# Kernel optimization log

Hardware: AMD Instinct MI355X
Metric: run time of the kernel (lower is better)

Reference implementation:

```python
import jax, jax.numpy as jnp
import numpy as np

OUT_DIM = 64
N_NODES = 50000
N_EDGES = 1000000


def setup_inputs() -> dict:
    key = jax.random.key(0)
    k1, k2, k3, k4, k5, k6 = jax.random.split(key, 6)
    return {
        "G_h": jax.random.normal(k1, (N_NODES, OUT_DIM), dtype=jnp.float32),
        "K_h": jax.random.normal(k2, (N_NODES, OUT_DIM), dtype=jnp.float32),
        "Q_h": jax.random.normal(k3, (N_NODES, OUT_DIM), dtype=jnp.float32),
        "V_h": jax.random.normal(k4, (N_NODES, 1, OUT_DIM), dtype=jnp.float32),
        "src": jax.random.randint(k5, (N_EDGES,), 0, N_NODES, dtype=jnp.int64),
        "dst": jax.random.randint(k6, (N_EDGES,), 0, N_NODES, dtype=jnp.int64),
    }


def reference(G_h, K_h, Q_h, V_h, src, dst):
    inv_sqrt_d = 1.0 / np.sqrt(OUT_DIM).astype(np.float32)
    # edge-wise gather of node features
    diff = G_h[src] - G_h[dst]                                   # [E, D]
    dist = -jnp.sqrt(jnp.sum(diff * diff, axis=-1) + 1e-6)       # [E]
    distance = jnp.exp(jnp.clip(dist * inv_sqrt_d, -5.0, 5.0))   # [E]
    score = jnp.sum(K_h[src] * Q_h[dst], axis=-1)                # [E]
    score_e = jnp.exp(jnp.clip(score * inv_sqrt_d, -5.0, 5.0))   # [E]
    weight = (score_e * distance)[:, None, None]                 # [E,1,1]
    v1_h = weight * V_h[src]                                     # [E,1,D]
    return v1_h
```

## Files before the change

### kernel.cpp

```cpp
#include <hip/hip_runtime.h>
#include <math.h>

#define N_NODES 50000
#define OUT_DIM 64

typedef float f32x4 __attribute__((ext_vector_type(4)));

__global__ __launch_bounds__(256) void edge_message_kernel(
    const float* __restrict__ G,
    const float* __restrict__ K,
    const float* __restrict__ Q,
    const float* __restrict__ V,
    const int* __restrict__ src,
    const int* __restrict__ dst,
    float* __restrict__ out,
    int nEdges)
{
    const int tid  = threadIdx.x;
    const int lane = tid & 63;
    const int grp  = lane >> 4;
    const int sub  = lane & 15;
    const int wavesPerBlock = blockDim.x >> 6;
    const int waveId = blockIdx.x * wavesPerBlock + (tid >> 6);
    const int waveStride = gridDim.x * wavesPerBlock;

    const f32x4* __restrict__ G4 = (const f32x4*)G;
    const f32x4* __restrict__ K4 = (const f32x4*)K;
    const f32x4* __restrict__ Q4 = (const f32x4*)Q;
    const f32x4* __restrict__ V4 = (const f32x4*)V;
    f32x4* __restrict__ out4 = (f32x4*)out;

    const float inv_sqrt_d = 0.125f;

    for (int base = waveId * 4; base < nEdges; base += waveStride * 4) {
        const int e = base + grp;
        const bool valid = (e < nEdges);
        const int ec = valid ? e : (nEdges - 1);

        const int s = __builtin_nontemporal_load(&src[ec]);
        const int d = __builtin_nontemporal_load(&dst[ec]);

        const f32x4 gs = G4[s * 16 + sub];
        const f32x4 gd = G4[d * 16 + sub];
        const f32x4 ks = K4[s * 16 + sub];
        const f32x4 qd = Q4[d * 16 + sub];
        const f32x4 vs = V4[s * 16 + sub];

        const f32x4 df = gs - gd;
        const f32x4 kq = ks * qd;
        float a = df.x * df.x + df.y * df.y + df.z * df.z + df.w * df.w;
        float b = kq.x + kq.y + kq.z + kq.w;

        #pragma unroll
        for (int off = 8; off > 0; off >>= 1) {
            a += __shfl_xor(a, off, 64);
            b += __shfl_xor(b, off, 64);
        }

        float t1 = -sqrtf(a + 1e-6f) * inv_sqrt_d;
        t1 = fminf(fmaxf(t1, -5.0f), 5.0f);
        float t2 = b * inv_sqrt_d;
        t2 = fminf(fmaxf(t2, -5.0f), 5.0f);
        const float w = __expf(t1 + t2);

        if (valid) {
            __builtin_nontemporal_store(w * vs, &out4[(size_t)e * 16 + sub]);
        }
    }
}

extern "C" void kernel_launch(void* const* d_in, const int* in_sizes, int n_in,
                              void* d_out, int out_size, void* d_ws, size_t ws_size,
                              hipStream_t stream)
{
    const float* G   = (const float*)d_in[0];
    const float* K   = (const float*)d_in[1];
    const float* Q   = (const float*)d_in[2];
    const float* V   = (const float*)d_in[3];
    const int*   src = (const int*)d_in[4];
    const int*   dst = (const int*)d_in[5];
    float* out = (float*)d_out;

    const int nEdges = in_sizes[4];

    const int block = 256;
    const int edgesPerBlock = (block / 64) * 4;
    int grid = (nEdges + edgesPerBlock - 1) / edgesPerBlock;
    if (grid > 2048) grid = 2048;

    edge_message_kernel<<<grid, block, 0, stream>>>(G, K, Q, V, src, dst, out, nEdges);
}
```

Before: 444.4 us.

## Process two edges per 16-lane group and prefetch next indices

Each 16-lane group now handles two edges per iteration, issuing ten gather loads before any reduction to raise memory-level parallelism. The src/dst indices for the next iteration are loaded ahead, so index-load latency overlaps with the current gathers. This uses more registers per thread and loads indices with regular rather than nontemporal loads, which could reduce occupancy. The grid is sized for eight edges per wave but is still capped at 2048 blocks.

New measurement: 441.2 us. No clear change (-0.7%).

```diff
diff --git a/kernel.cpp b/kernel.cpp
--- a/kernel.cpp
+++ b/kernel.cpp
@@ -23,6 +23,7 @@
     const int wavesPerBlock = blockDim.x >> 6;
     const int waveId = blockIdx.x * wavesPerBlock + (tid >> 6);
     const int waveStride = gridDim.x * wavesPerBlock;
+    const int iterEdges = waveStride * 8;
 
     const f32x4* __restrict__ G4 = (const f32x4*)G;
     const f32x4* __restrict__ K4 = (const f32x4*)K;
@@ -31,41 +32,75 @@
     f32x4* __restrict__ out4 = (f32x4*)out;
 
     const float inv_sqrt_d = 0.125f;
+    const int last = nEdges - 1;
 
-    for (int base = waveId * 4; base < nEdges; base += waveStride * 4) {
-        const int e = base + grp;
-        const bool valid = (e < nEdges);
-        const int ec = valid ? e : (nEdges - 1);
+    int base = waveId * 8;
+    if (base >= nEdges) return;
 
-        const int s = __builtin_nontemporal_load(&src[ec]);
-        const int d = __builtin_nontemporal_load(&dst[ec]);
+    int e0 = base + grp * 2;
+    int e1 = e0 + 1;
+    int s0 = src[min(e0, last)], d0 = dst[min(e0, last)];
+    int s1 = src[min(e1, last)], d1 = dst[min(e1, last)];
 
-        const f32x4 gs = G4[s * 16 + sub];
-        const f32x4 gd = G4[d * 16 + sub];
-        const f32x4 ks = K4[s * 16 + sub];
-        const f32x4 qd = Q4[d * 16 + sub];
-        const f32x4 vs = V4[s * 16 + sub];
+    for (; base < nEdges; base += iterEdges) {
+        e0 = base + grp * 2;
+        e1 = e0 + 1;
+        const bool v0 = (e0 < nEdges);
+        const bool v1 = (e1 < nEdges);
 
-        const f32x4 df = gs - gd;
-        const f32x4 kq = ks * qd;
-        float a = df.x * df.x + df.y * df.y + df.z * df.z + df.w * df.w;
-        float b = kq.x + kq.y + kq.z + kq.w;
+        const f32x4 gs0 = G4[s0 * 16 + sub];
+        const f32x4 gd0 = G4[d0 * 16 + sub];
+        const f32x4 ks0 = K4[s0 * 16 + sub];
+        const f32x4 qd0 = Q4[d0 * 16 + sub];
+        const f32x4 vs0 = V4[s0 * 16 + sub];
+        const f32x4 gs1 = G4[s1 * 16 + sub];
+        const f32x4 gd1 = G4[d1 * 16 + sub];
+        const f32x4 ks1 = K4[s1 * 16 + sub];
+        const f32x4 qd1 = Q4[d1 * 16 + sub];
+        const f32x4 vs1 = V4[s1 * 16 + sub];
 
-        #pragma unroll
-        for (int off = 8; off > 0; off >>= 1) {
-            a += __shfl_xor(a, off, 64);
-            b += __shfl_xor(b, off, 64);
+        const int nb = base + iterEdges;
+        const int ne0 = min(nb + grp * 2, last);
+        const int ne1 = min(nb + grp * 2 + 1, last);
+        const int ns0 = src[ne0], nd0 = dst[ne0];
+        const int ns1 = src[ne1], nd1 = dst[ne1];
+
+        {
+            const f32x4 df = gs0 - gd0;
+            const f32x4 kq = ks0 * qd0;
+            float a = df.x * df.x + df.y * df.y + df.z * df.z + df.w * df.w;
+            float b = kq.x + kq.y + kq.z + kq.w;
+            #pragma unroll
+            for (int off = 8; off > 0; off >>= 1) {
+                a += __shfl_xor(a, off, 64);
+                b += __shfl_xor(b, off, 64);
+            }
+            float t1 = -sqrtf(a + 1e-6f) * inv_sqrt_d;
+            t1 = fminf(fmaxf(t1, -5.0f), 5.0f);
+            float t2 = b * inv_sqrt_d;
+            t2 = fminf(fmaxf(t2, -5.0f), 5.0f);
+            const float w = __expf(t1 + t2);
+            if (v0) __builtin_nontemporal_store(w * vs0, &out4[(size_t)e0 * 16 + sub]);
+        }
+        {
+            const f32x4 df = gs1 - gd1;
+            const f32x4 kq = ks1 * qd1;
+            float a = df.x * df.x + df.y * df.y + df.z * df.z + df.w * df.w;
+            float b = kq.x + kq.y + kq.z + kq.w;
+            #pragma unroll
+            for (int off = 8; off > 0; off >>= 1) {
+                a += __shfl_xor(a, off, 64);
+                b += __shfl_xor(b, off, 64);
+            }
+            float t1 = -sqrtf(a + 1e-6f) * inv_sqrt_d;
+            t1 = fminf(fmaxf(t1, -5.0f), 5.0f);
+            float t2 = b * inv_sqrt_d;
+            t2 = fminf(fmaxf(t2, -5.0f), 5.0f);
+            const float w = __expf(t1 + t2);
+            if (v1) __builtin_nontemporal_store(w * vs1, &out4[(size_t)e1 * 16 + sub]);
         }
 
-        float t1 = -sqrtf(a + 1e-6f) * inv_sqrt_d;
-        t1 = fminf(fmaxf(t1, -5.0f), 5.0f);
-        float t2 = b * inv_sqrt_d;
-        t2 = fminf(fmaxf(t2, -5.0f), 5.0f);
-        const float w = __expf(t1 + t2);
-
-        if (valid) {
-            __builtin_nontemporal_store(w * vs, &out4[(size_t)e * 16 + sub]);
-        }
+        s0 = ns0; d0 = nd0; s1 = ns1; d1 = nd1;
     }
 }
 
@@ -84,7 +119,7 @@
     const int nEdges = in_sizes[4];
 
     const int block = 256;
-    const int edgesPerBlock = (block / 64) * 4;
+    const int edgesPerBlock = (block / 64) * 8;
     int grid = (nEdges + edgesPerBlock - 1) / edgesPerBlock;
     if (grid > 2048) grid = 2048;
 
```

## Bucket edges by source node to improve gather locality

Applied to the files above, without the earlier changes.

Adds a counting-sort pipeline (histogram, scan, scatter) that groups edges into buckets by src>>8, then runs the message kernel over the reordered edges and writes results back through a permutation. The goal is better cache locality for the src-indexed gathers of G, K and V. In exchange it adds four extra kernel launches, extra index traffic, and output writes that are scattered instead of sequential.

Result: no change. 442.7 us (-0.4%).

```diff
diff --git a/kernel.cpp b/kernel.cpp
--- a/kernel.cpp
+++ b/kernel.cpp
@@ -1,20 +1,103 @@
 #include <hip/hip_runtime.h>
 #include <math.h>
 
-#define N_NODES 50000
-#define OUT_DIM 64
+typedef float f32x4 __attribute__((ext_vector_type(4)));
 
-typedef float f32x4 __attribute__((ext_vector_type(4)));
+#define MAXNB 256
+#define BSHIFT 8
+#define UNROLL 8
+
+
+__global__ void zero_kernel(int* p, int n) {
+    int i = blockIdx.x * blockDim.x + threadIdx.x;
+    if (i < n) p[i] = 0;
+}
+
+__global__ __launch_bounds__(256) void hist_kernel(
+    const int* __restrict__ src, int nE, int nb, int* __restrict__ counts)
+{
+    __shared__ int lc[MAXNB];
+    for (int i = threadIdx.x; i < nb; i += blockDim.x) lc[i] = 0;
+    __syncthreads();
+    for (int e = blockIdx.x * blockDim.x + threadIdx.x; e < nE;
+         e += gridDim.x * blockDim.x)
+        atomicAdd(&lc[src[e] >> BSHIFT], 1);
+    __syncthreads();
+    for (int i = threadIdx.x; i < nb; i += blockDim.x) {
+        int c = lc[i];
+        if (c) atomicAdd(&counts[i], c);
+    }
+}
+
+__global__ __launch_bounds__(256) void scan_kernel(
+    const int* __restrict__ counts, int nb, int* __restrict__ cursor)
+{
+    __shared__ int buf[MAXNB];
+    int t = threadIdx.x;
+    int v = (t < nb) ? counts[t] : 0;
+    buf[t] = v;
+    __syncthreads();
+    #pragma unroll
+    for (int off = 1; off < MAXNB; off <<= 1) {
+        int x = (t >= off) ? buf[t - off] : 0;
+        __syncthreads();
+        buf[t] += x;
+        __syncthreads();
+    }
+    if (t < nb) cursor[t] = buf[t] - v;
+}
+
+__global__ __launch_bounds__(256) void scatter_kernel(
+    const int* __restrict__ src, const int* __restrict__ dst, int nE, int nb,
+    int* __restrict__ cursor, int* __restrict__ perm,
+    int* __restrict__ ssrc, int* __restrict__ sdst)
+{
+    __shared__ int lc[MAXNB];
+    __shared__ int lb[MAXNB];
+    const int chunkSize = blockDim.x * UNROLL;
+    for (int chunk = blockIdx.x * chunkSize; chunk < nE;
+         chunk += gridDim.x * chunkSize) {
+        for (int i = threadIdx.x; i < nb; i += blockDim.x) lc[i] = 0;
+        __syncthreads();
+        int myb[UNROLL], myoff[UNROLL], mys[UNROLL], myd[UNROLL];
+        #pragma unroll
+        for (int u = 0; u < UNROLL; u++) {
+            int e = chunk + u * blockDim.x + threadIdx.x;
+            if (e < nE) {
+                int s = src[e];
+                mys[u] = s; myd[u] = dst[e];
+                myb[u] = s >> BSHIFT;
+                myoff[u] = atomicAdd(&lc[myb[u]], 1);
+            } else myb[u] = -1;
+        }
+        __syncthreads();
+        for (int i = threadIdx.x; i < nb; i += blockDim.x) {
+            int c = lc[i];
+            lb[i] = c ? atomicAdd(&cursor[i], c) : 0;
+        }
+        __syncthreads();
+        #pragma unroll
+        for (int u = 0; u < UNROLL; u++) {
+            if (myb[u] >= 0) {
+                int pos = lb[myb[u]] + myoff[u];
+                int e = chunk + u * blockDim.x + threadIdx.x;
+                perm[pos] = e; ssrc[pos] = mys[u]; sdst[pos] = myd[u];
+            }
+        }
+        __syncthreads();
+    }
+}
 
 __global__ __launch_bounds__(256) void edge_message_kernel(
     const float* __restrict__ G,
     const float* __restrict__ K,
     const float* __restrict__ Q,
     const float* __restrict__ V,
-    const int* __restrict__ src,
-    const int* __restrict__ dst,
+    const int* __restrict__ perm,
+    const int* __restrict__ ssrc,
+    const int* __restrict__ sdst,
     float* __restrict__ out,
-    int nEdges)
+    int nE)
 {
     const int tid  = threadIdx.x;
     const int lane = tid & 63;
@@ -31,14 +114,16 @@
     f32x4* __restrict__ out4 = (f32x4*)out;
 
     const float inv_sqrt_d = 0.125f;
+    const int last = nE - 1;
 
-    for (int base = waveId * 4; base < nEdges; base += waveStride * 4) {
-        const int e = base + grp;
-        const bool valid = (e < nEdges);
-        const int ec = valid ? e : (nEdges - 1);
+    for (int i0 = waveId * 4; i0 < nE; i0 += waveStride * 4) {
+        const int i = i0 + grp;
+        const bool valid = (i < nE);
+        const int ic = valid ? i : last;
 
-        const int s = __builtin_nontemporal_load(&src[ec]);
-        const int d = __builtin_nontemporal_load(&dst[ec]);
+        const int s = ssrc[ic];
+        const int d = sdst[ic];
+        const int o = perm[ic];
 
         const f32x4 gs = G4[s * 16 + sub];
         const f32x4 gd = G4[d * 16 + sub];
@@ -64,7 +149,7 @@
         const float w = __expf(t1 + t2);
 
         if (valid) {
-            __builtin_nontemporal_store(w * vs, &out4[(size_t)e * 16 + sub]);
+            __builtin_nontemporal_store(w * vs, &out4[(size_t)o * 16 + sub]);
         }
     }
 }
@@ -81,12 +166,31 @@
     const int*   dst = (const int*)d_in[5];
     float* out = (float*)d_out;
 
-    const int nEdges = in_sizes[4];
+    const int nE = in_sizes[4];
+    const int nNodes = in_sizes[0] / 64;
+    const int nb = (nNodes + ((1 << BSHIFT) - 1)) >> BSHIFT;
 
-    const int block = 256;
-    const int edgesPerBlock = (block / 64) * 4;
-    int grid = (nEdges + edgesPerBlock - 1) / edgesPerBlock;
-    if (grid > 2048) grid = 2048;
+    int* counts = (int*)d_ws;
+    int* cursor = counts + 256;
+    int* perm   = cursor + 256;
+    int* ssrc   = perm + nE;
+    int* sdst   = ssrc + nE;
 
-    edge_message_kernel<<<grid, block, 0, stream>>>(G, K, Q, V, src, dst, out, nEdges);
+    zero_kernel<<<2, 256, 0, stream>>>(counts, 512);
+    hist_kernel<<<256, 256, 0, stream>>>(src, nE, nb, counts);
+    scan_kernel<<<1, 256, 0, stream>>>(counts, nb, cursor);
+    {
+        const int chunk = 256 * UNROLL;
+        int grid = (nE + chunk - 1) / chunk;
+        scatter_kernel<<<grid, 256, 0, stream>>>(src, dst, nE, nb,
+                                                 cursor, perm, ssrc, sdst);
+    }
+    {
+        const int block = 256;
+        const int edgesPerBlock = (block / 64) * 4;
+        int grid = (nE + edgesPerBlock - 1) / edgesPerBlock;
+        if (grid > 2048) grid = 2048;
+        edge_message_kernel<<<grid, block, 0, stream>>>(G, K, Q, V,
+                                                        perm, ssrc, sdst, out, nE);
+    }
 }
```
